# Kernel tuning notes

Measured on AMD Instinct MI355X. Metric: run time of the kernel, lower is better.

The kernel has to match this reference:

```python
import jax, jax.numpy as jnp
import numpy as np

N = 262144        # 64^3 grid unknowns
NNZ = 7 * N       # ~7-point stencil sparsity
BS = 32


def setup_inputs() -> dict:
    key = jax.random.key(0)
    k1, k2, k3, k4, k5 = jax.random.split(key, 5)
    y_pred = jax.random.normal(k1, (BS, N), dtype=jnp.float32)
    y_true = jax.random.normal(k2, (BS, N), dtype=jnp.float32)
    A_vals = jax.random.normal(k3, (NNZ,), dtype=jnp.float32)
    A_rows = jax.random.randint(k4, (NNZ,), 0, N, dtype=jnp.int32)
    A_cols = jax.random.randint(k5, (NNZ,), 0, N, dtype=jnp.int32)
    return {"y_pred": y_pred, "y_true": y_true, "A_vals": A_vals,
            "A_rows": A_rows, "A_cols": A_cols}


def reference(y_pred, y_true, A_vals, A_rows, A_cols):
    # YhatY[b] = <y_true[b], y_pred[b]>
    YhatY = jnp.sum(y_true * y_pred, axis=1)                      # (bs,)
    # Sparse matvec per batch: YhatAt = (A @ y_pred.T).T, COO form.
    # gathered[e, b] = A_vals[e] * y_pred[b, A_cols[e]]
    gathered = (y_pred[:, A_cols] * A_vals).T                     # (nnz, bs)
    YhatAt = jax.ops.segment_sum(gathered, A_rows, num_segments=N).T  # (bs, N)
    # YhatYhatAt[b] = <y_pred[b], A y_pred[b]>
    YhatYhatAt = jnp.sum(y_pred * YhatAt, axis=1)                 # (bs,)
    # diag(YhatY / YhatYhatAt) @ YhatAt == row-wise scale by alpha
    alpha = YhatY / YhatYhatAt                                    # (bs,)
    resid = y_true - alpha[:, None] * YhatAt                      # (bs, N)
    return jnp.mean(jnp.sum(resid * resid, axis=1))
```

## Files before the change

### kernel.cpp

```cpp
#include <hip/hip_runtime.h>

#define NGRID 262144
#define NNZ_C 1835008
#define TP    260
#define NS    256
#define TPAD  260


__global__ __launch_bounds__(256) void k_prep(
        const float* __restrict__ yp, float* __restrict__ yp_t,
        float* __restrict__ yat_t) {
    __shared__ __align__(16) float T[32 * TP];
    const int tid = threadIdx.x;
    const int l = tid & 63, w = tid >> 6;
    const size_t n0 = (size_t)blockIdx.x * 256;
    #pragma unroll
    for (int s = 0; s < 8; ++s) {
        const int b = s * 4 + w;
        const float4 a = *(const float4*)(yp + (size_t)b * NGRID + n0 + 4 * l);
        *(float4*)(&T[b * TP + 4 * l]) = a;
    }
    __syncthreads();
    float4* dst4 = (float4*)(yp_t + n0 * 32);
    float4* yat4 = (float4*)(yat_t + n0 * 32);
    #pragma unroll
    for (int q = 0; q < 8; ++q) {
        const int f = q * 256 + tid;
        const int n = f >> 3;
        const int bb = 4 * (f & 7);
        float4 v;
        v.x = T[(bb + 0) * TP + n];
        v.y = T[(bb + 1) * TP + n];
        v.z = T[(bb + 2) * TP + n];
        v.w = T[(bb + 3) * TP + n];
        dst4[f] = v;
        yat4[f] = make_float4(0.f, 0.f, 0.f, 0.f);
    }
}

__global__ void k_scatter(const float* __restrict__ vals,
                          const int* __restrict__ rows,
                          const int* __restrict__ cols,
                          const float* __restrict__ yp_t,
                          float* __restrict__ yat_t) {
    const size_t tid = (size_t)blockIdx.x * blockDim.x + threadIdx.x;
    const int b = (int)(tid & 31);
    const size_t e = tid >> 5;
    const float v = vals[e];
    const int r = rows[e];
    const int c = cols[e];
    const float x = yp_t[(size_t)c * 32 + b];
    atomicAdd(&yat_t[(size_t)r * 32 + b], v * x);
}

__global__ __launch_bounds__(256) void k_post(
        const float* __restrict__ yat_t, const float* __restrict__ yp,
        const float* __restrict__ yt, float* __restrict__ p2) {
    __shared__ __align__(16) float T[32 * TPAD];
    const int tid = threadIdx.x;
    const int g = blockIdx.x;
    const size_t n0 = (size_t)g * NS;
    const float4* yat4 = (const float4*)(yat_t + n0 * 32);
    #pragma unroll
    for (int q = 0; q < 8; ++q) {
        const int f = q * 256 + tid;
        const int n = f >> 3;
        const int b0 = 4 * (f & 7);
        const float4 v = yat4[f];
        T[(b0 + 0) * TPAD + n] = v.x;
        T[(b0 + 1) * TPAD + n] = v.y;
        T[(b0 + 2) * TPAD + n] = v.z;
        T[(b0 + 3) * TPAD + n] = v.w;
    }
    __syncthreads();
    const int b = tid >> 3, j = tid & 7;
    const float* ytb = yt + (size_t)b * NGRID + n0;
    const float* ypb = yp + (size_t)b * NGRID + n0;
    const float* Tb = &T[b * TPAD];
    float c1 = 0.f, c2 = 0.f, c3 = 0.f, st = 0.f, sy = 0.f;
    #pragma unroll
    for (int s = 0; s < NS / 32; ++s) {
        const int n = 4 * j + 32 * s;
        const float4 a = *(const float4*)(Tb + n);
        const float4 t = *(const float4*)(ytb + n);
        const float4 p = *(const float4*)(ypb + n);
        c1 = fmaf(p.x, a.x, c1); c2 = fmaf(t.x, a.x, c2);
        c3 = fmaf(a.x, a.x, c3); st = fmaf(t.x, t.x, st);
        sy = fmaf(t.x, p.x, sy);
        c1 = fmaf(p.y, a.y, c1); c2 = fmaf(t.y, a.y, c2);
        c3 = fmaf(a.y, a.y, c3); st = fmaf(t.y, t.y, st);
        sy = fmaf(t.y, p.y, sy);
        c1 = fmaf(p.z, a.z, c1); c2 = fmaf(t.z, a.z, c2);
        c3 = fmaf(a.z, a.z, c3); st = fmaf(t.z, t.z, st);
        sy = fmaf(t.z, p.z, sy);
        c1 = fmaf(p.w, a.w, c1); c2 = fmaf(t.w, a.w, c2);
        c3 = fmaf(a.w, a.w, c3); st = fmaf(t.w, t.w, st);
        sy = fmaf(t.w, p.w, sy);
    }
    #pragma unroll
    for (int d = 4; d; d >>= 1) {
        c1 += __shfl_down(c1, d, 8);
        c2 += __shfl_down(c2, d, 8);
        c3 += __shfl_down(c3, d, 8);
        st += __shfl_down(st, d, 8);
        sy += __shfl_down(sy, d, 8);
    }
    if (j == 0) {
        float* row = p2 + (size_t)g * 160;
        row[0 * 32 + b] = c1;
        row[1 * 32 + b] = c2;
        row[2 * 32 + b] = c3;
        row[3 * 32 + b] = st;
        row[4 * 32 + b] = sy;
    }
}

__global__ __launch_bounds__(256) void k_finish1(
        const float* __restrict__ p2, float* __restrict__ pr2) {
    const int tid = threadIdx.x, g = blockIdx.x;
    if (tid < 160) {
        float acc = 0.f;
        #pragma unroll
        for (int j = 0; j < 32; ++j) acc += p2[(size_t)(g * 32 + j) * 160 + tid];
        pr2[g * 160 + tid] = acc;
    }
}

__global__ __launch_bounds__(256) void k_finish2(
        const float* __restrict__ pr2, float* __restrict__ out) {
    __shared__ float tot[160];
    __shared__ float lb[32];
    const int tid = threadIdx.x;
    if (tid < 160) {
        float acc = 0.f;
        #pragma unroll
        for (int j = 0; j < 32; ++j) acc += pr2[j * 160 + tid];
        tot[tid] = acc;
    }
    __syncthreads();
    if (tid < 32) {
        const float c1 = tot[0 + tid];
        const float c2 = tot[32 + tid];
        const float c3 = tot[64 + tid];
        const float stt = tot[96 + tid];
        const float sty = tot[128 + tid];
        const float a = sty / c1;
        lb[tid] = fmaf(a * a, c3, fmaf(-2.f * a, c2, stt));
    }
    __syncthreads();
    if (tid == 0) {
        float s = 0.f;
        #pragma unroll
        for (int i = 0; i < 32; ++i) s += lb[i];
        out[0] = s * (1.0f / 32.0f);
    }
}

extern "C" void kernel_launch(void* const* d_in, const int* in_sizes, int n_in,
                              void* d_out, int out_size, void* d_ws, size_t ws_size,
                              hipStream_t stream) {
    const float* yp = (const float*)d_in[0];
    const float* yt = (const float*)d_in[1];
    const float* Av = (const float*)d_in[2];
    const int*   Ar = (const int*)d_in[3];
    const int*   Ac = (const int*)d_in[4];
    float* out = (float*)d_out;

    float* ws    = (float*)d_ws;
    float* yp_t  = ws;
    float* yat_t = yp_t + (size_t)NGRID * 32;
    float* p2    = yat_t + (size_t)NGRID * 32;
    float* pr2   = p2 + 1024 * 160;

    k_prep<<<1024, 256, 0, stream>>>(yp, yp_t, yat_t);
    k_scatter<<<(NNZ_C * 32) / 256, 256, 0, stream>>>(Av, Ar, Ac, yp_t, yat_t);
    k_post<<<1024, 256, 0, stream>>>(yat_t, yp, yt, p2);
    k_finish1<<<32, 256, 0, stream>>>(p2, pr2);
    k_finish2<<<1, 256, 0, stream>>>(pr2, out);
}
```

Baseline: 323.4 us.

## Pack two fixed-point partial sums into 64-bit integer atomics in scatter

```diff
diff --git a/kernel.cpp b/kernel.cpp
--- a/kernel.cpp
+++ b/kernel.cpp
@@ -5,6 +5,9 @@
 #define TP    260
 #define NS    256
 #define TPAD  260
+
+#define FPSCALE   524288.0f
+#define FPINV     (1.0f / 524288.0f)
 
 
 __global__ __launch_bounds__(256) void k_prep(
@@ -42,35 +45,43 @@
                           const int* __restrict__ rows,
                           const int* __restrict__ cols,
                           const float* __restrict__ yp_t,
-                          float* __restrict__ yat_t) {
+                          unsigned long long* __restrict__ yat64) {
     const size_t tid = (size_t)blockIdx.x * blockDim.x + threadIdx.x;
-    const int b = (int)(tid & 31);
-    const size_t e = tid >> 5;
+    const int b2 = (int)(tid & 15);
+    const size_t e = tid >> 4;
     const float v = vals[e];
     const int r = rows[e];
     const int c = cols[e];
-    const float x = yp_t[(size_t)c * 32 + b];
-    atomicAdd(&yat_t[(size_t)r * 32 + b], v * x);
+    const float2 x2 = *(const float2*)(yp_t + (size_t)c * 32 + 2 * b2);
+    const long long i0 = (long long)__float2int_rn(v * x2.x * FPSCALE);
+    const long long i1 = (long long)__float2int_rn(v * x2.y * FPSCALE);
+    const unsigned long long pk = (unsigned long long)((i1 << 32) + i0);
+    atomicAdd(&yat64[(size_t)r * 16 + b2], pk);
 }
 
 __global__ __launch_bounds__(256) void k_post(
-        const float* __restrict__ yat_t, const float* __restrict__ yp,
-        const float* __restrict__ yt, float* __restrict__ p2) {
+        const unsigned long long* __restrict__ yat64,
+        const float* __restrict__ yp, const float* __restrict__ yt,
+        float* __restrict__ p2) {
     __shared__ __align__(16) float T[32 * TPAD];
     const int tid = threadIdx.x;
     const int g = blockIdx.x;
     const size_t n0 = (size_t)g * NS;
-    const float4* yat4 = (const float4*)(yat_t + n0 * 32);
+    const ulonglong2* y2 = (const ulonglong2*)(yat64 + n0 * 16);
     #pragma unroll
     for (int q = 0; q < 8; ++q) {
         const int f = q * 256 + tid;
         const int n = f >> 3;
         const int b0 = 4 * (f & 7);
-        const float4 v = yat4[f];
-        T[(b0 + 0) * TPAD + n] = v.x;
-        T[(b0 + 1) * TPAD + n] = v.y;
-        T[(b0 + 2) * TPAD + n] = v.z;
-        T[(b0 + 3) * TPAD + n] = v.w;
+        const ulonglong2 pv = y2[f];
+        const int lo0 = (int)(unsigned)pv.x;
+        const int hi0 = (int)((pv.x + 0x80000000ULL) >> 32);
+        const int lo1 = (int)(unsigned)pv.y;
+        const int hi1 = (int)((pv.y + 0x80000000ULL) >> 32);
+        T[(b0 + 0) * TPAD + n] = (float)lo0 * FPINV;
+        T[(b0 + 1) * TPAD + n] = (float)hi0 * FPINV;
+        T[(b0 + 2) * TPAD + n] = (float)lo1 * FPINV;
+        T[(b0 + 3) * TPAD + n] = (float)hi1 * FPINV;
     }
     __syncthreads();
     const int b = tid >> 3, j = tid & 7;
@@ -168,13 +179,14 @@
 
     float* ws    = (float*)d_ws;
     float* yp_t  = ws;
-    float* yat_t = yp_t + (size_t)NGRID * 32;
-    float* p2    = yat_t + (size_t)NGRID * 32;
+    float* yat_f = yp_t + (size_t)NGRID * 32;
+    unsigned long long* yat64 = (unsigned long long*)yat_f;
+    float* p2    = yat_f + (size_t)NGRID * 32;
     float* pr2   = p2 + 1024 * 160;
 
-    k_prep<<<1024, 256, 0, stream>>>(yp, yp_t, yat_t);
-    k_scatter<<<(NNZ_C * 32) / 256, 256, 0, stream>>>(Av, Ar, Ac, yp_t, yat_t);
-    k_post<<<1024, 256, 0, stream>>>(yat_t, yp, yt, p2);
+    k_prep<<<1024, 256, 0, stream>>>(yp, yp_t, yat_f);
+    k_scatter<<<(NNZ_C * 16) / 256, 256, 0, stream>>>(Av, Ar, Ac, yp_t, yat64);
+    k_post<<<1024, 256, 0, stream>>>(yat64, yp, yt, p2);
     k_finish1<<<32, 256, 0, stream>>>(p2, pr2);
     k_finish2<<<1, 256, 0, stream>>>(pr2, out);
 }
```

Result: faster. 298.4 us (-7.7%).
